# Optimization experiments

Measured on AMD Instinct MI355X. Metric: run time of the kernel, lower is better.

Reference implementation:

```python
import jax, jax.numpy as jnp
import numpy as np

NC = 80            # number of classes (COCO)
NM = 32            # mask coefficients (YOLOv5-seg)
D = 4 + 1 + NC + NM
N_ANCHORS = 100800  # 1280x1280 input, strides 8/16/32, 3 anchors
CONF_THRES = 0.25
IOU_THRES = 0.45
MAX_DET = 300
TOPK = 4096        # fixed pre-NMS candidate budget (jit-compatible stand-in for boolean filter)


def setup_inputs() -> dict:
    key = jax.random.key(0)
    x = jax.random.uniform(key, (1, N_ANCHORS, D), dtype=jnp.float32)
    return {"x": x}


def _pairwise_iou(boxes):
    # boxes: [K, 4] in (y1, x1, y2, x2)
    y1, x1, y2, x2 = boxes[:, 0], boxes[:, 1], boxes[:, 2], boxes[:, 3]
    area = (y2 - y1) * (x2 - x1)
    iy1 = jnp.maximum(y1[:, None], y1[None, :])
    ix1 = jnp.maximum(x1[:, None], x1[None, :])
    iy2 = jnp.minimum(y2[:, None], y2[None, :])
    ix2 = jnp.minimum(x2[:, None], x2[None, :])
    inter = jnp.clip(iy2 - iy1, 0.0) * jnp.clip(ix2 - ix1, 0.0)
    union = area[:, None] + area[None, :] - inter
    return inter / jnp.maximum(union, 1e-9)


def reference(x):
    p = x[0]                                   # [N, D] (loop returns after first image)
    obj = p[:, 4]
    valid = obj > CONF_THRES                   # candidates = obj score > conf_thres
    cls_scores = p[:, 5:5 + NC] * obj[:, None] # scores = cls * obj
    scores = jnp.max(cls_scores, axis=1)
    classes = jnp.argmax(cls_scores, axis=1).astype(x.dtype)
    # xywh (center) -> yxyx
    xc, yc, w, h = p[:, 0], p[:, 1], p[:, 2], p[:, 3]
    yxyx = jnp.stack([yc - h * 0.5, xc - w * 0.5, yc + h * 0.5, xc + w * 0.5], axis=1)
    masks = p[:, 5 + NC:]                      # [N, NM]
    # replace torch's boolean-filter gather with fixed-size top-K over masked scores
    scores_m = jnp.where(valid, scores, -1.0)
    top_s, top_i = jax.lax.top_k(scores_m, TOPK)   # sorted desc, as torchvision nms requires
    b = yxyx[top_i]                            # [K, 4]
    keep0 = top_s > -0.5                       # only real candidates
    iou = _pairwise_iou(b)                     # [K, K]
    j_idx = jnp.arange(TOPK)

    def body(i, keep):
        sup = keep[i] & (iou[i] > IOU_THRES) & (j_idx > i)
        return keep & ~sup

    keep = jax.lax.fori_loop(0, TOPK, body, keep0)
    # pad/select top MAX_DET surviving detections (score -1.0 marks padding)
    sel_s = jnp.where(keep, top_s, -1.0)
    out_s, out_i = jax.lax.top_k(sel_s, MAX_DET)
    gi = top_i[out_i]
    return (yxyx[gi][None], classes[gi][None], out_s[None], masks[gi][None])
```

## Files before the change

### kernel.cpp

```cpp
#include <hip/hip_runtime.h>


#define AS1 __attribute__((address_space(1)))
#define AS3 __attribute__((address_space(3)))

constexpr int    N_ANCH = 100800;
constexpr int    DIMV   = 117;
constexpr int    NCLS   = 80;
constexpr int    TOPKN  = 4096;
constexpr int    MAXDET = 300;
constexpr int    KCAP   = 12288;
constexpr int    NBUCK  = 16384;
constexpr int    NSLICE = 32;

constexpr size_t WS_HIST   = 0;
constexpr size_t WS_SCORES = WS_HIST   + 65536ull * 4;
constexpr size_t WS_CLS    = WS_SCORES + 100800ull * 4;
constexpr size_t WS_SEL    = WS_CLS    + 100800ull * 4;
constexpr size_t WS_KEYS   = WS_SEL    + 256;
constexpr size_t WS_RANK   = WS_KEYS   + (size_t)KCAP * 8;
constexpr size_t WS_SIDX   = WS_RANK   + (size_t)KCAP * 4;
constexpr size_t WS_SSC    = WS_SIDX   + 4096ull * 4;
constexpr size_t WS_BOXES  = WS_SSC    + 4096ull * 4;
constexpr size_t WS_MASK   = WS_BOXES  + 4096ull * 16;
constexpr size_t WS_OUTI   = WS_MASK   + 4096ull * 64 * 8;
constexpr size_t WS_OUTS   = WS_OUTI   + 1200;

__global__ void zero_kernel(unsigned* __restrict__ slices, int* __restrict__ sel,
                            int* __restrict__ rank) {
    int i = blockIdx.x * blockDim.x + threadIdx.x;
    if (i < NSLICE * NBUCK) slices[i] = 0u;
    if (i < KCAP)           rank[i]  = 0;
    if (i < 64)             sel[i]   = 0;
}

constexpr int SROWS = 64;
__global__ void score_kernel(const float* __restrict__ x, float* __restrict__ scores,
                             int* __restrict__ cls, unsigned* __restrict__ slices) {
    __shared__ float sx[SROWS * DIMV];
    int block0 = blockIdx.x * SROWS;
    const float4* src = (const float4*)(x + (size_t)block0 * DIMV);
    float4* dst = (float4*)sx;
    constexpr int NV4 = SROWS * DIMV / 4;
    for (int i = threadIdx.x; i < NV4; i += 128) dst[i] = src[i];
    __syncthreads();
    int row  = threadIdx.x >> 1;
    int half = threadIdx.x & 1;
    const float* rp = sx + row * DIMV;
    float obj = rp[4];
    const float* cp = rp + 5 + half * 40;
    float best = -1.0f;
    int   bc   = half * 40;
#pragma unroll 8
    for (int c = 0; c < 40; ++c) {
        float s = __fmul_rn(cp[c], obj);
        if (s > best) { best = s; bc = half * 40 + c; }
    }
    float so = __shfl_xor(best, 1);
    int   co = __shfl_xor(bc, 1);
    if (half == 0) {
        if (so > best) { best = so; bc = co; }
        int a = block0 + row;
        bool valid = obj > 0.25f;
        scores[a] = valid ? best : -1.0f;
        cls[a]    = bc;
        if (valid) {
            unsigned b = __float_as_uint(best) >> 16;
            atomicAdd(&slices[(blockIdx.x & (NSLICE - 1)) * NBUCK + b], 1u);
        }
    }
}

__global__ void reduce_hist_kernel(const unsigned* __restrict__ slices,
                                   unsigned* __restrict__ hist) {
    int b = blockIdx.x * 256 + threadIdx.x;
    unsigned s = 0;
#pragma unroll
    for (int k = 0; k < NSLICE; ++k) s += slices[k * NBUCK + b];
    hist[b] = s;
}

__global__ void select_kernel(const unsigned* __restrict__ hist, int* sel) {
    __shared__ unsigned sv[1024];
    int t = threadIdx.x;
    int base = NBUCK - 16 * (t + 1);
    const uint4* hp = (const uint4*)(hist + base);
    unsigned own = 0;
#pragma unroll
    for (int k = 0; k < 4; ++k) {
        uint4 v = hp[k];
        own += v.x + v.y + v.z + v.w;
    }
    sv[t] = own;
    __syncthreads();
    for (int off = 1; off < 1024; off <<= 1) {
        unsigned v = (t >= off) ? sv[t - off] : 0u;
        __syncthreads();
        sv[t] += v;
        __syncthreads();
    }
    unsigned incl = sv[t];
    unsigned before = incl - own;
    if (before < (unsigned)TOPKN && incl >= (unsigned)TOPKN) {
        unsigned running = before;
        for (int k = 15; k >= 0; --k) {
            unsigned h = hist[base + k];
            running += h;
            if (running >= (unsigned)TOPKN) {
                sel[0] = base + k;
                sel[1] = (int)(running - h);
                break;
            }
        }
    }
}

__global__ void compact_kernel(const float* __restrict__ scores, int* sel,
                               unsigned long long* __restrict__ keys) {
    int a = blockIdx.x * blockDim.x + threadIdx.x;
    if (a >= N_ANCH) return;
    float s = scores[a];
    if (s < 0.0f) return;
    unsigned bits = __float_as_uint(s);
    if ((int)(bits >> 16) < sel[0]) return;
    int pos = atomicAdd(&sel[2], 1);
    if (pos < KCAP) keys[pos] = ((unsigned long long)bits << 32) | (unsigned)(~a);
}

constexpr int NCOLP = 4;
__global__ void rank_kernel(const unsigned long long* __restrict__ keys,
                            const int* __restrict__ sel, int* __restrict__ rank) {
    __shared__ unsigned long long tile[2048];
    int n = sel[2]; if (n > KCAP) n = KCAP;
    int i = blockIdx.x * 256 + threadIdx.x;
    unsigned long long myKey = (i < n) ? keys[i] : 0ull;
    int cnt = 0;
    for (int t0 = blockIdx.y * 2048; t0 < n; t0 += 2048 * NCOLP) {
        int m = n - t0; if (m > 2048) m = 2048;
        for (int j = threadIdx.x; j < m; j += 256) tile[j] = keys[t0 + j];
        __syncthreads();
        int j = 0;
        for (; j + 3 < m; j += 4) {
            cnt += (tile[j]     > myKey);
            cnt += (tile[j + 1] > myKey);
            cnt += (tile[j + 2] > myKey);
            cnt += (tile[j + 3] > myKey);
        }
        for (; j < m; ++j) cnt += (tile[j] > myKey);
        __syncthreads();
    }
    if (i < n && cnt < TOPKN) atomicAdd(&rank[i], cnt);
}

__global__ void scatter_kernel(const float* __restrict__ x,
                               const unsigned long long* __restrict__ keys,
                               const int* __restrict__ sel, const int* __restrict__ rank,
                               int* __restrict__ sidx, float* __restrict__ sscore,
                               float* __restrict__ boxes) {
    int n = sel[2]; if (n > KCAP) n = KCAP;
    int i = blockIdx.x * 256 + threadIdx.x;
    if (i >= n) return;
    int r = rank[i];
    if (r >= TOPKN) return;
    unsigned long long k = keys[i];
    int a = (int)(~(unsigned)(k & 0xFFFFFFFFull));
    sidx[r]   = a;
    sscore[r] = __uint_as_float((unsigned)(k >> 32));
    const float* p = x + (size_t)a * DIMV;
    float xc = p[0], yc = p[1], w = p[2], h = p[3];
    float hw = __fmul_rn(w, 0.5f);
    float hh = __fmul_rn(h, 0.5f);
    boxes[r * 4 + 0] = __fsub_rn(yc, hh);
    boxes[r * 4 + 1] = __fsub_rn(xc, hw);
    boxes[r * 4 + 2] = __fadd_rn(yc, hh);
    boxes[r * 4 + 3] = __fadd_rn(xc, hw);
}

__global__ void iou_mask_kernel(const float* __restrict__ boxes,
                                unsigned long long* __restrict__ mask) {
    int colT = blockIdx.x, rowT = blockIdx.y;
    int t = threadIdx.x;
    int r = rowT * 64 + t;
    if (colT < rowT) {
        mask[(size_t)r * 64 + colT] = 0ull;
        return;
    }
    __shared__ float cb[64][5];
    int cj = colT * 64 + t;
    {
        float y1 = boxes[cj * 4 + 0], x1 = boxes[cj * 4 + 1];
        float y2 = boxes[cj * 4 + 2], x2 = boxes[cj * 4 + 3];
        cb[t][0] = y1; cb[t][1] = x1; cb[t][2] = y2; cb[t][3] = x2;
        cb[t][4] = __fmul_rn(__fsub_rn(y2, y1), __fsub_rn(x2, x1));
    }
    __syncthreads();
    float ry1 = boxes[r * 4 + 0], rx1 = boxes[r * 4 + 1];
    float ry2 = boxes[r * 4 + 2], rx2 = boxes[r * 4 + 3];
    float rarea = __fmul_rn(__fsub_rn(ry2, ry1), __fsub_rn(rx2, rx1));
    unsigned long long bitsw = 0ull;
#pragma unroll 8
    for (int j = 0; j < 64; ++j) {
        float iy1 = fmaxf(ry1, cb[j][0]);
        float ix1 = fmaxf(rx1, cb[j][1]);
        float iy2 = fminf(ry2, cb[j][2]);
        float ix2 = fminf(rx2, cb[j][3]);
        float ih = fmaxf(__fsub_rn(iy2, iy1), 0.0f);
        float iw = fmaxf(__fsub_rn(ix2, ix1), 0.0f);
        float inter = __fmul_rn(ih, iw);
        float uni = __fsub_rn(__fadd_rn(rarea, cb[j][4]), inter);
        float iou = __fdiv_rn(inter, fmaxf(uni, 1e-9f));
        if (iou > 0.45f && (colT * 64 + j) > r) bitsw |= (1ull << j);
    }
    mask[(size_t)r * 64 + colT] = bitsw;
}

__global__ void __launch_bounds__(64, 1)
nms_scan_kernel(const unsigned long long* __restrict__ mask,
                const float* __restrict__ sscore,
                int* __restrict__ outIdx, float* __restrict__ outScore) {
    int lane = threadIdx.x;
    unsigned long long remv = 0ull;
    __shared__ __align__(16) unsigned long long tile[2 * 4096];
    __shared__ int keepArr[MAXDET];
    __shared__ unsigned long long remvFinal[64];
    int count = 0;

    auto issueBatch = [&](int w) {
        const char* gbase = (const char*)mask + (size_t)w * 32768 + (size_t)lane * 16;
        char* lbase = (char*)tile + (size_t)(w & 1) * 32768;
#pragma unroll
        for (int i = 0; i < 32; ++i) {
            __builtin_amdgcn_global_load_lds(
                (AS1 const unsigned*)(gbase + (size_t)i * 1024),
                (AS3 unsigned*)(lbase + (size_t)i * 1024), 16, 0, 0);
        }
    };

    issueBatch(0);
    for (int w = 0; w < 64 && count < MAXDET; ++w) {
        if (w + 1 < 64) issueBatch(w + 1);
        unsigned long long cand = __shfl(~remv, w);
        if (!cand) continue;
        asm volatile("s_waitcnt vmcnt(32)" ::: "memory");
        const unsigned long long* trow = tile + (size_t)(w & 1) * 4096;
        while (cand && count < MAXDET) {
            int bs[8];
            unsigned long long c2 = cand;
            int g = 0;
#pragma unroll
            for (int t = 0; t < 8; ++t) {
                bs[t] = c2 ? (int)__builtin_ctzll(c2) : 0;
                if (c2) { c2 &= c2 - 1; g = t + 1; }
            }
            unsigned long long mvs[8];
#pragma unroll
            for (int t = 0; t < 8; ++t) {
                mvs[t] = trow[(size_t)bs[t] * 64 + lane];
            }
#pragma unroll
            for (int t = 0; t < 8; ++t) {
                if (t < g && count < MAXDET) {
                    int b = bs[t];
                    unsigned long long bal = __ballot(((remv >> b) & 1ull) != 0);
                    if (!((bal >> w) & 1ull)) {
                        if (lane == 0) keepArr[count] = (w << 6) + b;
                        count++;
                        remv |= mvs[t];
                    }
                }
            }
            cand = c2;
        }
    }
    __syncthreads();
    remvFinal[lane] = remv;
    __syncthreads();
    int K = count;
    for (int k = lane; k < K; k += 64) {
        int s = keepArr[k];
        outIdx[k] = s;
        outScore[k] = sscore[s];
    }
    if (K < MAXDET && lane == 0) {
        int filled = K;
        for (int w = 0; w < 64 && filled < MAXDET; ++w) {
            unsigned long long word = remvFinal[w];
            while (word && filled < MAXDET) {
                int b = (int)__builtin_ctzll(word);
                word &= word - 1;
                outIdx[filled] = (w << 6) + b;
                outScore[filled] = -1.0f;
                filled++;
            }
        }
    }
}

__global__ void write_out_kernel(const float* __restrict__ x, const int* __restrict__ sidx,
                                 const int* __restrict__ cls, const float* __restrict__ boxes,
                                 const int* __restrict__ outIdx, const float* __restrict__ outScore,
                                 float* __restrict__ out) {
    int o = blockIdx.x;
    int t = threadIdx.x;
    int s = outIdx[o];
    int a = sidx[s];
    if (t < 32) {
        out[1800 + o * 32 + t] = x[(size_t)a * DIMV + 85 + t];
    } else if (t < 36) {
        out[o * 4 + (t - 32)] = boxes[s * 4 + (t - 32)];
    } else if (t == 36) {
        out[1200 + o] = (float)cls[a];
    } else if (t == 37) {
        out[1500 + o] = outScore[o];
    }
}

extern "C" void kernel_launch(void* const* d_in, const int* in_sizes, int n_in,
                              void* d_out, int out_size, void* d_ws, size_t ws_size,
                              hipStream_t stream) {
    const float* x = (const float*)d_in[0];
    char* ws = (char*)d_ws;
    unsigned*            hist   = (unsigned*)(ws + WS_HIST);
    float*               scores = (float*)(ws + WS_SCORES);
    int*                 cls    = (int*)(ws + WS_CLS);
    int*                 sel    = (int*)(ws + WS_SEL);
    unsigned long long*  keys   = (unsigned long long*)(ws + WS_KEYS);
    int*                 rank   = (int*)(ws + WS_RANK);
    int*                 sidx   = (int*)(ws + WS_SIDX);
    float*               sscore = (float*)(ws + WS_SSC);
    float*               boxes  = (float*)(ws + WS_BOXES);
    unsigned long long*  mask   = (unsigned long long*)(ws + WS_MASK);
    unsigned*            slices = (unsigned*)(ws + WS_MASK);
    int*                 outIdx = (int*)(ws + WS_OUTI);
    float*               outSc  = (float*)(ws + WS_OUTS);

    zero_kernel<<<(NSLICE * NBUCK + 255) / 256, 256, 0, stream>>>(slices, sel, rank);
    score_kernel<<<N_ANCH / SROWS, 128, 0, stream>>>(x, scores, cls, slices);
    reduce_hist_kernel<<<NBUCK / 256, 256, 0, stream>>>(slices, hist);
    select_kernel<<<1, 1024, 0, stream>>>(hist, sel);
    compact_kernel<<<(N_ANCH + 255) / 256, 256, 0, stream>>>(scores, sel, keys);
    dim3 rg(KCAP / 256, NCOLP);
    rank_kernel<<<rg, 256, 0, stream>>>(keys, sel, rank);
    scatter_kernel<<<KCAP / 256, 256, 0, stream>>>(x, keys, sel, rank, sidx, sscore, boxes);
    dim3 mg(64, 64);
    iou_mask_kernel<<<mg, 64, 0, stream>>>(boxes, mask);
    nms_scan_kernel<<<1, 64, 0, stream>>>(mask, sscore, outIdx, outSc);
    write_out_kernel<<<MAXDET, 64, 0, stream>>>(x, sidx, cls, boxes, outIdx, outSc, (float*)d_out);
}
```

Baseline: 216.9 us.

## Prefetch candidate mask rows directly from global in NMS scan

```diff
diff --git a/kernel.cpp b/kernel.cpp
--- a/kernel.cpp
+++ b/kernel.cpp
@@ -1,8 +1,5 @@
 #include <hip/hip_runtime.h>
 
-
-#define AS1 __attribute__((address_space(1)))
-#define AS3 __attribute__((address_space(3)))
 
 constexpr int    N_ANCH = 100800;
 constexpr int    DIMV   = 117;
@@ -220,59 +217,64 @@
                 int* __restrict__ outIdx, float* __restrict__ outScore) {
     int lane = threadIdx.x;
     unsigned long long remv = 0ull;
-    __shared__ __align__(16) unsigned long long tile[2 * 4096];
     __shared__ int keepArr[MAXDET];
     __shared__ unsigned long long remvFinal[64];
     int count = 0;
 
-    auto issueBatch = [&](int w) {
-        const char* gbase = (const char*)mask + (size_t)w * 32768 + (size_t)lane * 16;
-        char* lbase = (char*)tile + (size_t)(w & 1) * 32768;
-#pragma unroll
-        for (int i = 0; i < 32; ++i) {
-            __builtin_amdgcn_global_load_lds(
-                (AS1 const unsigned*)(gbase + (size_t)i * 1024),
-                (AS3 unsigned*)(lbase + (size_t)i * 1024), 16, 0, 0);
+    int curWord = -1;
+    unsigned long long candRem = 0ull;
+
+    auto fetchGroup = [&](int* bs, int& g) {
+        g = 0;
+#pragma unroll
+        for (int t = 0; t < 8; ++t) {
+            if (candRem == 0ull) {
+                while (curWord < 63) {
+                    ++curWord;
+                    candRem = __shfl(~remv, curWord);
+                    if (candRem) break;
+                }
+            }
+            if (candRem) {
+                int b = (int)__builtin_ctzll(candRem);
+                candRem &= candRem - 1;
+                bs[t] = (curWord << 6) + b;
+                g = t + 1;
+            } else {
+                bs[t] = 0;
+            }
         }
     };
 
-    issueBatch(0);
-    for (int w = 0; w < 64 && count < MAXDET; ++w) {
-        if (w + 1 < 64) issueBatch(w + 1);
-        unsigned long long cand = __shfl(~remv, w);
-        if (!cand) continue;
-        asm volatile("s_waitcnt vmcnt(32)" ::: "memory");
-        const unsigned long long* trow = tile + (size_t)(w & 1) * 4096;
-        while (cand && count < MAXDET) {
-            int bs[8];
-            unsigned long long c2 = cand;
-            int g = 0;
-#pragma unroll
-            for (int t = 0; t < 8; ++t) {
-                bs[t] = c2 ? (int)__builtin_ctzll(c2) : 0;
-                if (c2) { c2 &= c2 - 1; g = t + 1; }
-            }
-            unsigned long long mvs[8];
-#pragma unroll
-            for (int t = 0; t < 8; ++t) {
-                mvs[t] = trow[(size_t)bs[t] * 64 + lane];
-            }
-#pragma unroll
-            for (int t = 0; t < 8; ++t) {
-                if (t < g && count < MAXDET) {
-                    int b = bs[t];
-                    unsigned long long bal = __ballot(((remv >> b) & 1ull) != 0);
-                    if (!((bal >> w) & 1ull)) {
-                        if (lane == 0) keepArr[count] = (w << 6) + b;
-                        count++;
-                        remv |= mvs[t];
-                    }
+    int bsA[8], gA;
+    unsigned long long mA[8];
+    fetchGroup(bsA, gA);
+#pragma unroll
+    for (int t = 0; t < 8; ++t) mA[t] = mask[(size_t)bsA[t] * 64 + lane];
+
+    while (gA > 0 && count < MAXDET) {
+        int bsB[8], gB;
+        unsigned long long mB[8];
+        fetchGroup(bsB, gB);
+#pragma unroll
+        for (int t = 0; t < 8; ++t) mB[t] = mask[(size_t)bsB[t] * 64 + lane];
+#pragma unroll
+        for (int t = 0; t < 8; ++t) {
+            if (t < gA && count < MAXDET) {
+                int r = bsA[t];
+                unsigned long long bal = __ballot(((remv >> (r & 63)) & 1ull) != 0);
+                if (!((bal >> (r >> 6)) & 1ull)) {
+                    if (lane == 0) keepArr[count] = r;
+                    count++;
+                    remv |= mA[t];
                 }
             }
-            cand = c2;
-        }
-    }
-    __syncthreads();
+        }
+        gA = gB;
+#pragma unroll
+        for (int t = 0; t < 8; ++t) { bsA[t] = bsB[t]; mA[t] = mB[t]; }
+    }
+
     remvFinal[lane] = remv;
     __syncthreads();
     int K = count;
```

After: 227.6 us. +4.9%, slower.
